# Kernel optimization log

Measured on AMD Instinct MI355X. Metric: run time of the kernel, lower is better.

## Reference

```python
import jax, jax.numpy as jnp
import numpy as np

DT = 0.01  # continuous-time step for the S4D/Vandermonde reservoir kernel


def setup_inputs() -> dict:
    key = jax.random.key(0)
    ks = jax.random.split(key, 10)
    B, H, L, N = 16, 128, 4096, 64
    u = jax.random.normal(ks[0], (B, H, L), dtype=jnp.float32)
    # stable diagonal SSM: real part of Lambda strictly negative
    lambda_re = -0.5 * jax.random.uniform(ks[1], (H, N), dtype=jnp.float32) - 0.1
    lambda_im = jax.random.normal(ks[2], (H, N), dtype=jnp.float32) * np.pi
    w_re = jax.random.normal(ks[3], (H, N), dtype=jnp.float32) / np.sqrt(N)
    w_im = jax.random.normal(ks[4], (H, N), dtype=jnp.float32) / np.sqrt(N)
    d = jax.random.normal(ks[5], (H,), dtype=jnp.float32)
    mlp_w1 = jax.random.normal(ks[6], (H, H), dtype=jnp.float32) / np.sqrt(H)
    mlp_b1 = jnp.zeros((H,), dtype=jnp.float32)
    mlp_w2 = jax.random.normal(ks[7], (H, H), dtype=jnp.float32) / np.sqrt(H)
    mlp_b2 = jnp.zeros((H,), dtype=jnp.float32)
    return {"u": u, "lambda_re": lambda_re, "lambda_im": lambda_im,
            "w_re": w_re, "w_im": w_im, "d": d,
            "mlp_w1": mlp_w1, "mlp_b1": mlp_b1,
            "mlp_w2": mlp_w2, "mlp_b2": mlp_b2}


def reference(u, lambda_re, lambda_im, w_re, w_im, d,
              mlp_w1, mlp_b1, mlp_w2, mlp_b2):
    B, H, L = u.shape
    Lam = lambda_re + 1j * lambda_im          # (H, N) diagonal state matrix
    W = w_re + 1j * w_im                      # (H, N) merged C*B readout
    ell = jnp.arange(L, dtype=jnp.float32)
    # Vandermonde kernel: K[h, l] = sum_n W[h,n] * exp(dt * Lambda[h,n] * l)
    V = jnp.exp((DT * Lam)[:, :, None] * ell[None, None, :])  # (H, N, L)
    K = jnp.einsum('hn,hnl->hl', W, V)                         # (H, L) complex
    # causal FFT convolution (pad to 2L to avoid circular wrap)
    n = 2 * L
    y = jnp.fft.ifft(jnp.fft.fft(u, n=n, axis=-1) * jnp.fft.fft(K, n=n, axis=-1)[None],
                     n=n, axis=-1)[..., :L]
    y = y + d[None, :, None] * u              # skip / feed-through term
    y = y.real                                # Real() projection
    # 1x1-conv MLP with ReLU (mlp_layers = 2)
    h1 = jax.nn.relu(jnp.einsum('oh,bhl->bol', mlp_w1, y) + mlp_b1[None, :, None])
    y2 = jax.nn.relu(jnp.einsum('oh,bhl->bol', mlp_w2, h1) + mlp_b2[None, :, None])
    return y2
```

## Files before the change

### kernel.cpp

```cpp
#include <hip/hip_runtime.h>
#include <hip/hip_bf16.h>

#define B_ 16
#define H_ 128
#define L_ 4096
#define N_ 64
#define DT_ 0.01f

typedef __bf16 bf16;
typedef __bf16 bf16x8 __attribute__((ext_vector_type(8)));
typedef __bf16 bf16x4 __attribute__((ext_vector_type(4)));
typedef float f32x4 __attribute__((ext_vector_type(4)));

__global__ __launch_bounds__(64) void k_prep(
        const float* __restrict__ lre, const float* __restrict__ lim,
        const float* __restrict__ wre, const float* __restrict__ wim,
        const float* __restrict__ w1, const float* __restrict__ w2,
        bf16* __restrict__ w1b, bf16* __restrict__ w2b,
        bf16* __restrict__ Pbf, bf16* __restrict__ Qbf,
        float* __restrict__ tap, float* __restrict__ acre, float* __restrict__ acim) {
    __shared__ bf16  Pl[128 * 72];
    __shared__ bf16  Ql[64 * 136];
    __shared__ float red[64 * 65];

    const int h = blockIdx.x, n = threadIdx.x;

    w1b[h * H_ + n]      = (bf16)w1[h * H_ + n];
    w1b[h * H_ + 64 + n] = (bf16)w1[h * H_ + 64 + n];
    w2b[h * H_ + n]      = (bf16)w2[h * H_ + n];
    w2b[h * H_ + 64 + n] = (bf16)w2[h * H_ + 64 + n];

    const float lr = lre[h * 64 + n] * DT_, li = lim[h * 64 + n] * DT_;
    const float e = expf(lr);
    const float ar = e * cosf(li), ai = e * sinf(li);
    const float wr = wre[h * 64 + n], wi = wim[h * 64 + n];
    const float war = wr * ar - wi * ai;
    const float wai = wr * ai + wi * ar;
    float pr = 1.f, pi = 0.f;
    for (int dlt = 0; dlt < 64; ++dlt) {
        Pl[n * 72 + (63 - dlt)]        = (bf16)pr;
        Pl[(64 + n) * 72 + (63 - dlt)] = (bf16)pi;
        Ql[dlt * 136 + 2 * n]     = (bf16)(war * pr - wai * pi);
        Ql[dlt * 136 + 2 * n + 1] = (bf16)(-(war * pi + wai * pr));
        red[dlt * 65 + n] = wr * pr - wi * pi;
        const float npr = ar * pr - ai * pi;
        const float npi = ar * pi + ai * pr;
        pr = npr; pi = npi;
    }
    acre[h * 64 + n] = pr;
    acim[h * 64 + n] = pi;
    __syncthreads();

    float s = 0.f;
    #pragma unroll
    for (int k = 0; k < 64; ++k) s += red[n * 65 + k];
    tap[h * 64 + n] = s;

    bf16* Ph = Pbf + (size_t)h * 128 * 64;
    bf16* Qh = Qbf + (size_t)h * 64 * 128;
    #pragma unroll
    for (int i = 0; i < 16; ++i) {
        const int flat = i * 512 + n * 8;
        {
            const int row = flat >> 6, col = flat & 63;
            *(bf16x8*)(Ph + flat) = *(const bf16x8*)(&Pl[row * 72 + col]);
        }
        {
            const int row = flat >> 7, col = flat & 127;
            *(bf16x8*)(Qh + flat) = *(const bf16x8*)(&Ql[row * 136 + col]);
        }
    }
}

#define USWZ(c, k) ((c) * 64 + (((((k) >> 4) ^ ((c) & 3)) << 4) | ((k) & 15)))
#define SSWZ(c, k) ((c) * 128 + (((((k) >> 4) ^ ((c) & 7)) << 4) | ((k) & 15)))
__global__ __launch_bounds__(512, 4) void k_ssm2(
        const float* __restrict__ u, const float* __restrict__ dv,
        const bf16* __restrict__ Pbf, const bf16* __restrict__ Qbf,
        const float* __restrict__ tap,
        const float* __restrict__ acre, const float* __restrict__ acim,
        bf16* __restrict__ ybf) {
    __shared__ bf16  Ubf[64 * 64];
    __shared__ float Ctr[128 * 65];
    __shared__ bf16  Sbf[64 * 128];
    __shared__ bf16  Tm[64 * 72];

    const int tid = threadIdx.x;
    const int bh  = blockIdx.x;
    const int h   = bh & (H_ - 1);
    const float* __restrict__ up = u + (size_t)bh * L_;

    {
        const int c = tid >> 3, j0 = (tid & 7) << 3;
        const float4* src = (const float4*)(up + c * 64 + j0);
        float4 f0 = src[0], f1 = src[1];
        bf16x8 t;
        t[0] = (bf16)f0.x; t[1] = (bf16)f0.y; t[2] = (bf16)f0.z; t[3] = (bf16)f0.w;
        t[4] = (bf16)f1.x; t[5] = (bf16)f1.y; t[6] = (bf16)f1.z; t[7] = (bf16)f1.w;
        *(bf16x8*)(&Ubf[USWZ(c, j0)]) = t;
    }
    {
        const int dlt = tid >> 3, j0 = (tid & 7) << 3;
        const float* tp = tap + h * 64;
        const float dh = dv[h];
        bf16x8 t;
        #pragma unroll
        for (int e = 0; e < 8; ++e) {
            const int j = j0 + e;
            float v = (j <= dlt) ? tp[dlt - j] : 0.f;
            if (j == dlt) v += dh;
            t[e] = (bf16)v;
        }
        *(bf16x8*)(&Tm[dlt * 72 + j0]) = t;
    }
    __syncthreads();

    const int lane = tid & 63, wv = tid >> 6;
    const int cl = lane & 15, q = lane >> 4;

    {
        f32x4 acc[4];
        #pragma unroll
        for (int nt = 0; nt < 4; ++nt) acc[nt] = (f32x4){0.f, 0.f, 0.f, 0.f};
        const bf16* Ph = Pbf + (size_t)h * 128 * 64;
        #pragma unroll
        for (int ks = 0; ks < 2; ++ks) {
            const int k0 = ks * 32 + q * 8;
            const bf16x8 a = *(const bf16x8*)(Ph + (size_t)(wv * 16 + cl) * 64 + k0);
            #pragma unroll
            for (int nt = 0; nt < 4; ++nt) {
                const int c = nt * 16 + cl;
                const bf16x8 bfr = *(const bf16x8*)(&Ubf[USWZ(c, k0)]);
                acc[nt] = __builtin_amdgcn_mfma_f32_16x16x32_bf16(a, bfr, acc[nt], 0, 0, 0);
            }
        }
        #pragma unroll
        for (int nt = 0; nt < 4; ++nt)
            #pragma unroll
            for (int r = 0; r < 4; ++r)
                Ctr[(wv * 16 + q * 4 + r) * 65 + nt * 16 + cl] = acc[nt][r];
    }
    __syncthreads();

    if (wv == 0) {
        const int n = lane;
        const float ar = acre[h * 64 + n], ai = acim[h * 64 + n];
        float sr = 0.f, si = 0.f;
        #pragma unroll 8
        for (int c = 0; c < 64; ++c) {
            bf16* sp = &Sbf[SSWZ(c, 2 * n)];
            sp[0] = (bf16)sr;
            sp[1] = (bf16)si;
            const float cr = Ctr[n * 65 + c];
            const float ci = Ctr[(64 + n) * 65 + c];
            const float nr = fmaf(ar, sr, fmaf(-ai, si, cr));
            const float ni = fmaf(ar, si, fmaf(ai, sr, ci));
            sr = nr; si = ni;
        }
    }
    __syncthreads();

    {
        const int mt  = wv >> 1;
        const int nt0 = (wv & 1) * 2;
        f32x4 acc[2];
        acc[0] = (f32x4){0.f, 0.f, 0.f, 0.f};
        acc[1] = (f32x4){0.f, 0.f, 0.f, 0.f};
        const bf16* Qh = Qbf + (size_t)h * 64 * 128;
        #pragma unroll
        for (int ks = 0; ks < 4; ++ks) {
            const int k0 = ks * 32 + q * 8;
            const bf16x8 a = *(const bf16x8*)(Qh + (size_t)(mt * 16 + cl) * 128 + k0);
            #pragma unroll
            for (int j = 0; j < 2; ++j) {
                const int c = (nt0 + j) * 16 + cl;
                const bf16x8 bfr = *(const bf16x8*)(&Sbf[SSWZ(c, k0)]);
                acc[j] = __builtin_amdgcn_mfma_f32_16x16x32_bf16(a, bfr, acc[j], 0, 0, 0);
            }
        }
        #pragma unroll
        for (int ks = 0; ks < 2; ++ks) {
            const int k0 = ks * 32 + q * 8;
            const bf16x8 a = *(const bf16x8*)(&Tm[(mt * 16 + cl) * 72 + k0]);
            #pragma unroll
            for (int j = 0; j < 2; ++j) {
                const int c = (nt0 + j) * 16 + cl;
                const bf16x8 bfr = *(const bf16x8*)(&Ubf[USWZ(c, k0)]);
                acc[j] = __builtin_amdgcn_mfma_f32_16x16x32_bf16(a, bfr, acc[j], 0, 0, 0);
            }
        }
        bf16* Yb = (bf16*)Ctr;
        #pragma unroll
        for (int j = 0; j < 2; ++j) {
            const int c = (nt0 + j) * 16 + cl;
            bf16x4 yv;
            #pragma unroll
            for (int r = 0; r < 4; ++r) yv[r] = (bf16)acc[j][r];
            *(bf16x4*)(&Yb[c * 72 + mt * 16 + q * 4]) = yv;
        }
    }
    __syncthreads();

    {
        const bf16* Yb = (const bf16*)Ctr;
        const int c = tid >> 3, s0 = (tid & 7) << 3;
        bf16x8 v = *(const bf16x8*)(&Yb[c * 72 + s0]);
        *(bf16x8*)(ybf + (size_t)bh * L_ + c * 64 + s0) = v;
    }
}

#define YSTR 136
__global__ __launch_bounds__(256, 4) void k_mlp(
        const bf16* __restrict__ ybf,
        const bf16* __restrict__ w1b, const bf16* __restrict__ w2b,
        const float* __restrict__ b1, const float* __restrict__ b2,
        float* __restrict__ out) {
    __shared__ float Ys[128 * 68];
    __shared__ float B1s[H_], B2s[H_];
    bf16* YT = (bf16*)Ys;

    const int tid = threadIdx.x;
    const int b   = blockIdx.x >> 6;
    const int lt  = blockIdx.x & 63;
    const int l0  = lt * 64;

    if (tid < H_) { B1s[tid] = b1[tid]; B2s[tid] = b2[tid]; }

    {
        const int h  = tid >> 1;
        const int lh = (tid & 1) * 32;
        const bf16x8* src = (const bf16x8*)(ybf + ((size_t)b * H_ + h) * L_ + l0 + lh);
        #pragma unroll
        for (int v = 0; v < 4; ++v) {
            bf16x8 d = src[v];
            #pragma unroll
            for (int e = 0; e < 8; ++e) YT[(lh + v * 8 + e) * YSTR + h] = d[e];
        }
    }
    __syncthreads();

    const int lane = tid & 63;
    const int wv   = tid >> 6;
    const int m    = lane & 15;
    const int q    = lane >> 4;
    const int m0   = wv * 32;

    f32x4 acc[2][4];
    #pragma unroll
    for (int i = 0; i < 2; ++i)
        #pragma unroll
        for (int nt = 0; nt < 4; ++nt) acc[i][nt] = (f32x4){0.f, 0.f, 0.f, 0.f};

    #pragma unroll
    for (int kb = 0; kb < 4; ++kb) {
        const bf16x8 a0 = *(const bf16x8*)(w1b + (size_t)(m0 + m)      * H_ + kb * 32 + q * 8);
        const bf16x8 a1 = *(const bf16x8*)(w1b + (size_t)(m0 + 16 + m) * H_ + kb * 32 + q * 8);
        #pragma unroll
        for (int nt = 0; nt < 4; ++nt) {
            const bf16x8 bfr = *(const bf16x8*)(&YT[(nt * 16 + m) * YSTR + kb * 32 + q * 8]);
            acc[0][nt] = __builtin_amdgcn_mfma_f32_16x16x32_bf16(a0, bfr, acc[0][nt], 0, 0, 0);
            acc[1][nt] = __builtin_amdgcn_mfma_f32_16x16x32_bf16(a1, bfr, acc[1][nt], 0, 0, 0);
        }
    }
    __syncthreads();

    #pragma unroll
    for (int i = 0; i < 2; ++i) {
        const int o0 = m0 + 16 * i + 4 * q;
        #pragma unroll
        for (int nt = 0; nt < 4; ++nt) {
            const f32x4 v = acc[i][nt];
            bf16x4 hv;
            #pragma unroll
            for (int r = 0; r < 4; ++r) {
                float x = v[r] + B1s[o0 + r];
                hv[r] = (bf16)fmaxf(x, 0.f);
            }
            *(bf16x4*)(&YT[(nt * 16 + m) * YSTR + o0]) = hv;
        }
    }
    __syncthreads();

    f32x4 acc2[2][4];
    #pragma unroll
    for (int i = 0; i < 2; ++i)
        #pragma unroll
        for (int nt = 0; nt < 4; ++nt) acc2[i][nt] = (f32x4){0.f, 0.f, 0.f, 0.f};

    #pragma unroll
    for (int kb = 0; kb < 4; ++kb) {
        const bf16x8 a0 = *(const bf16x8*)(w2b + (size_t)(m0 + m)      * H_ + kb * 32 + q * 8);
        const bf16x8 a1 = *(const bf16x8*)(w2b + (size_t)(m0 + 16 + m) * H_ + kb * 32 + q * 8);
        #pragma unroll
        for (int nt = 0; nt < 4; ++nt) {
            const bf16x8 bfr = *(const bf16x8*)(&YT[(nt * 16 + m) * YSTR + kb * 32 + q * 8]);
            acc2[0][nt] = __builtin_amdgcn_mfma_f32_16x16x32_bf16(a0, bfr, acc2[0][nt], 0, 0, 0);
            acc2[1][nt] = __builtin_amdgcn_mfma_f32_16x16x32_bf16(a1, bfr, acc2[1][nt], 0, 0, 0);
        }
    }
    __syncthreads();

    #pragma unroll
    for (int i = 0; i < 2; ++i) {
        const int o0 = m0 + 16 * i + 4 * q;
        #pragma unroll
        for (int nt = 0; nt < 4; ++nt) {
            const f32x4 v = acc2[i][nt];
            #pragma unroll
            for (int r = 0; r < 4; ++r) {
                float x = v[r] + B2s[o0 + r];
                Ys[(o0 + r) * 68 + nt * 16 + m] = fmaxf(x, 0.f);
            }
        }
    }
    __syncthreads();

    {
        const int rg = tid >> 4, c4 = (tid & 15) << 2;
        float* op = out + ((size_t)b * H_) * L_ + l0;
        #pragma unroll
        for (int v = 0; v < 8; ++v) {
            const int row = v * 16 + rg;
            const float4 val = *(const float4*)(&Ys[row * 68 + c4]);
            *(float4*)(op + (size_t)row * L_ + c4) = val;
        }
    }
}

extern "C" void kernel_launch(void* const* d_in, const int* in_sizes, int n_in,
                              void* d_out, int out_size, void* d_ws, size_t ws_size,
                              hipStream_t stream) {
    const float* u   = (const float*)d_in[0];
    const float* lre = (const float*)d_in[1];
    const float* lim = (const float*)d_in[2];
    const float* wre = (const float*)d_in[3];
    const float* wim = (const float*)d_in[4];
    const float* dv  = (const float*)d_in[5];
    const float* w1  = (const float*)d_in[6];
    const float* b1  = (const float*)d_in[7];
    const float* w2  = (const float*)d_in[8];
    const float* b2  = (const float*)d_in[9];
    float* out = (float*)d_out;

    char* ws = (char*)d_ws;
    bf16*  ybf  = (bf16*)ws;                 ws += (size_t)B_ * H_ * L_ * 2;
    bf16*  w1b  = (bf16*)ws;                 ws += H_ * H_ * 2;
    bf16*  w2b  = (bf16*)ws;                 ws += H_ * H_ * 2;
    bf16*  Pbf  = (bf16*)ws;                 ws += (size_t)H_ * 128 * 64 * 2;
    bf16*  Qbf  = (bf16*)ws;                 ws += (size_t)H_ * 64 * 128 * 2;
    float* tap  = (float*)ws;                ws += H_ * 64 * 4;
    float* acre = (float*)ws;                ws += H_ * 64 * 4;
    float* acim = (float*)ws;                ws += H_ * 64 * 4;

    hipLaunchKernelGGL(k_prep, dim3(H_), dim3(64), 0, stream,
                       lre, lim, wre, wim, w1, w2, w1b, w2b,
                       Pbf, Qbf, tap, acre, acim);
    hipLaunchKernelGGL(k_ssm2, dim3(B_ * H_), dim3(512), 0, stream,
                       u, dv, Pbf, Qbf, tap, acre, acim, ybf);
    hipLaunchKernelGGL(k_mlp, dim3(B_ * (L_ / 64)), dim3(256), 0, stream,
                       ybf, w1b, w2b, b1, b2, out);
}
```

Baseline: 138.1 us.

## Fuse SSM prep into main kernel, compute power matrices in registers, loop over batches

Removes the separate k_prep launch. The Vandermonde P/Q fragments, taps and A^64 are now computed directly in registers and shared memory with closed-form exp/sin/cos instead of serial powers. Each block now handles 4 batch elements for one head, so the setup cost is paid once per block, and the bf16 weight conversion is folded into the same kernel. This cuts a launch and the workspace traffic. In exchange the grid shrinks from 2048 to 512 blocks, a serial loop is added per block, and fast-math intrinsics may lose some accuracy.

Result: faster. 131.2 us (-5.0%).

```diff
diff --git a/kernel.cpp b/kernel.cpp
--- a/kernel.cpp
+++ b/kernel.cpp
@@ -12,200 +12,210 @@
 typedef __bf16 bf16x4 __attribute__((ext_vector_type(4)));
 typedef float f32x4 __attribute__((ext_vector_type(4)));
 
-__global__ __launch_bounds__(64) void k_prep(
+#define USWZ(c, k) ((c) * 64 + (((((k) >> 4) ^ ((c) & 3)) << 4) | ((k) & 15)))
+#define SSWZ(c, k) ((c) * 128 + (((((k) >> 4) ^ ((c) & 7)) << 4) | ((k) & 15)))
+
+__global__ __launch_bounds__(512, 4) void k_ssm3(
+        const float* __restrict__ u,
         const float* __restrict__ lre, const float* __restrict__ lim,
         const float* __restrict__ wre, const float* __restrict__ wim,
+        const float* __restrict__ dv,
         const float* __restrict__ w1, const float* __restrict__ w2,
         bf16* __restrict__ w1b, bf16* __restrict__ w2b,
-        bf16* __restrict__ Pbf, bf16* __restrict__ Qbf,
-        float* __restrict__ tap, float* __restrict__ acre, float* __restrict__ acim) {
-    __shared__ bf16  Pl[128 * 72];
-    __shared__ bf16  Ql[64 * 136];
-    __shared__ float red[64 * 65];
-
-    const int h = blockIdx.x, n = threadIdx.x;
-
-    w1b[h * H_ + n]      = (bf16)w1[h * H_ + n];
-    w1b[h * H_ + 64 + n] = (bf16)w1[h * H_ + 64 + n];
-    w2b[h * H_ + n]      = (bf16)w2[h * H_ + n];
-    w2b[h * H_ + 64 + n] = (bf16)w2[h * H_ + 64 + n];
-
-    const float lr = lre[h * 64 + n] * DT_, li = lim[h * 64 + n] * DT_;
-    const float e = expf(lr);
-    const float ar = e * cosf(li), ai = e * sinf(li);
-    const float wr = wre[h * 64 + n], wi = wim[h * 64 + n];
-    const float war = wr * ar - wi * ai;
-    const float wai = wr * ai + wi * ar;
-    float pr = 1.f, pi = 0.f;
-    for (int dlt = 0; dlt < 64; ++dlt) {
-        Pl[n * 72 + (63 - dlt)]        = (bf16)pr;
-        Pl[(64 + n) * 72 + (63 - dlt)] = (bf16)pi;
-        Ql[dlt * 136 + 2 * n]     = (bf16)(war * pr - wai * pi);
-        Ql[dlt * 136 + 2 * n + 1] = (bf16)(-(war * pi + wai * pr));
-        red[dlt * 65 + n] = wr * pr - wi * pi;
-        const float npr = ar * pr - ai * pi;
-        const float npi = ar * pi + ai * pr;
-        pr = npr; pi = npi;
-    }
-    acre[h * 64 + n] = pr;
-    acim[h * 64 + n] = pi;
-    __syncthreads();
-
-    float s = 0.f;
-    #pragma unroll
-    for (int k = 0; k < 64; ++k) s += red[n * 65 + k];
-    tap[h * 64 + n] = s;
-
-    bf16* Ph = Pbf + (size_t)h * 128 * 64;
-    bf16* Qh = Qbf + (size_t)h * 64 * 128;
-    #pragma unroll
-    for (int i = 0; i < 16; ++i) {
-        const int flat = i * 512 + n * 8;
-        {
-            const int row = flat >> 6, col = flat & 63;
-            *(bf16x8*)(Ph + flat) = *(const bf16x8*)(&Pl[row * 72 + col]);
-        }
-        {
-            const int row = flat >> 7, col = flat & 127;
-            *(bf16x8*)(Qh + flat) = *(const bf16x8*)(&Ql[row * 136 + col]);
-        }
-    }
-}
-
-#define USWZ(c, k) ((c) * 64 + (((((k) >> 4) ^ ((c) & 3)) << 4) | ((k) & 15)))
-#define SSWZ(c, k) ((c) * 128 + (((((k) >> 4) ^ ((c) & 7)) << 4) | ((k) & 15)))
-__global__ __launch_bounds__(512, 4) void k_ssm2(
-        const float* __restrict__ u, const float* __restrict__ dv,
-        const bf16* __restrict__ Pbf, const bf16* __restrict__ Qbf,
-        const float* __restrict__ tap,
-        const float* __restrict__ acre, const float* __restrict__ acim,
         bf16* __restrict__ ybf) {
-    __shared__ bf16  Ubf[64 * 64];
-    __shared__ float Ctr[128 * 65];
-    __shared__ bf16  Sbf[64 * 128];
-    __shared__ bf16  Tm[64 * 72];
-
-    const int tid = threadIdx.x;
-    const int bh  = blockIdx.x;
-    const int h   = bh & (H_ - 1);
-    const float* __restrict__ up = u + (size_t)bh * L_;
-
-    {
-        const int c = tid >> 3, j0 = (tid & 7) << 3;
-        const float4* src = (const float4*)(up + c * 64 + j0);
-        float4 f0 = src[0], f1 = src[1];
-        bf16x8 t;
-        t[0] = (bf16)f0.x; t[1] = (bf16)f0.y; t[2] = (bf16)f0.z; t[3] = (bf16)f0.w;
-        t[4] = (bf16)f1.x; t[5] = (bf16)f1.y; t[6] = (bf16)f1.z; t[7] = (bf16)f1.w;
-        *(bf16x8*)(&Ubf[USWZ(c, j0)]) = t;
-    }
+    alignas(16) __shared__ char smem[68352];
+    bf16*  Ubf  = (bf16*)smem;
+    float* Ctr  = (float*)(smem + 8192);
+    bf16*  Sbf  = (bf16*)(smem + 41472);
+    bf16*  Tm   = (bf16*)(smem + 57856);
+    float* lamS = (float*)(smem + 67072);
+    float* taps = (float*)(smem + 68096);
+
+    const int tid  = threadIdx.x;
+    const int lane = tid & 63, wv = tid >> 6;
+    const int cl   = lane & 15, q = lane >> 4;
+    const int bId  = blockIdx.x;
+    const int h    = bId & 127;
+    const int bg   = bId >> 7;
+
+    if (tid < 64) {
+        if (bId < 256) w1b[bId * 64 + tid] = (bf16)w1[bId * 64 + tid];
+        else           w2b[(bId - 256) * 64 + tid] = (bf16)w2[(bId - 256) * 64 + tid];
+    }
+    if (tid < 64) {
+        lamS[tid]       = lre[h * 64 + tid] * DT_;
+        lamS[64 + tid]  = lim[h * 64 + tid] * DT_;
+        lamS[128 + tid] = wre[h * 64 + tid];
+        lamS[192 + tid] = wim[h * 64 + tid];
+    }
+    __syncthreads();
+
+    bf16x8 pA0, pA1;
+    {
+        const int row = wv * 16 + cl;
+        const int n = row & 63;
+        const bool isIm = row >= 64;
+        const float lr = lamS[n], li = lamS[64 + n];
+        #pragma unroll
+        for (int jj = 0; jj < 8; ++jj) {
+            const float p0 = (float)(63 - (q * 8 + jj));
+            const float e0 = __expf(p0 * lr);
+            pA0[jj] = (bf16)(isIm ? e0 * __sinf(p0 * li) : e0 * __cosf(p0 * li));
+            const float p1 = (float)(63 - (32 + q * 8 + jj));
+            const float e1 = __expf(p1 * lr);
+            pA1[jj] = (bf16)(isIm ? e1 * __sinf(p1 * li) : e1 * __cosf(p1 * li));
+        }
+    }
+    bf16x8 qA[4];
+    {
+        const float fd = (float)((wv >> 1) * 16 + cl + 1);
+        #pragma unroll
+        for (int ks = 0; ks < 4; ++ks) {
+            #pragma unroll
+            for (int nn = 0; nn < 4; ++nn) {
+                const int n = ks * 16 + q * 4 + nn;
+                const float lr = lamS[n], li = lamS[64 + n];
+                const float wr = lamS[128 + n], wi = lamS[192 + n];
+                const float e  = __expf(fd * lr);
+                const float cr = e * __cosf(fd * li), ci = e * __sinf(fd * li);
+                qA[ks][2 * nn]     = (bf16)(wr * cr - wi * ci);
+                qA[ks][2 * nn + 1] = (bf16)(-(wr * ci + wi * cr));
+            }
+        }
+    }
+    float a64r, a64i;
+    {
+        const float lr = lamS[lane], li = lamS[64 + lane];
+        const float e = __expf(64.f * lr);
+        a64r = e * __cosf(64.f * li);
+        a64i = e * __sinf(64.f * li);
+    }
+    {
+        const float lr = lamS[lane], li = lamS[64 + lane];
+        const float wr = lamS[128 + lane], wi = lamS[192 + lane];
+        #pragma unroll
+        for (int i = 0; i < 8; ++i) {
+            const int dlt = wv * 8 + i;
+            const float fd = (float)dlt;
+            const float e = __expf(fd * lr);
+            float t = wr * e * __cosf(fd * li) - wi * e * __sinf(fd * li);
+            #pragma unroll
+            for (int d = 1; d < 64; d <<= 1) t += __shfl_xor(t, d, 64);
+            if (lane == 0) taps[dlt] = t;
+        }
+    }
+    __syncthreads();
+
     {
         const int dlt = tid >> 3, j0 = (tid & 7) << 3;
-        const float* tp = tap + h * 64;
         const float dh = dv[h];
         bf16x8 t;
         #pragma unroll
         for (int e = 0; e < 8; ++e) {
             const int j = j0 + e;
-            float v = (j <= dlt) ? tp[dlt - j] : 0.f;
+            float v = (j <= dlt) ? taps[dlt - j] : 0.f;
             if (j == dlt) v += dh;
             t[e] = (bf16)v;
         }
         *(bf16x8*)(&Tm[dlt * 72 + j0]) = t;
     }
-    __syncthreads();
-
-    const int lane = tid & 63, wv = tid >> 6;
-    const int cl = lane & 15, q = lane >> 4;
-
-    {
-        f32x4 acc[4];
-        #pragma unroll
-        for (int nt = 0; nt < 4; ++nt) acc[nt] = (f32x4){0.f, 0.f, 0.f, 0.f};
-        const bf16* Ph = Pbf + (size_t)h * 128 * 64;
-        #pragma unroll
-        for (int ks = 0; ks < 2; ++ks) {
-            const int k0 = ks * 32 + q * 8;
-            const bf16x8 a = *(const bf16x8*)(Ph + (size_t)(wv * 16 + cl) * 64 + k0);
+
+    const int mt = wv >> 1, nt0 = (wv & 1) * 2;
+    for (int it = 0; it < 4; ++it) {
+        const int bh = (bg * 4 + it) * 128 + h;
+        const float* __restrict__ up = u + (size_t)bh * L_;
+
+        {
+            const int c = tid >> 3, j0 = (tid & 7) << 3;
+            const float4* src = (const float4*)(up + c * 64 + j0);
+            const float4 f0 = src[0], f1 = src[1];
+            bf16x8 t;
+            t[0] = (bf16)f0.x; t[1] = (bf16)f0.y; t[2] = (bf16)f0.z; t[3] = (bf16)f0.w;
+            t[4] = (bf16)f1.x; t[5] = (bf16)f1.y; t[6] = (bf16)f1.z; t[7] = (bf16)f1.w;
+            *(bf16x8*)(&Ubf[USWZ(c, j0)]) = t;
+        }
+        __syncthreads();
+
+        {
+            f32x4 acc[4];
+            #pragma unroll
+            for (int nt = 0; nt < 4; ++nt) acc[nt] = (f32x4){0.f, 0.f, 0.f, 0.f};
             #pragma unroll
             for (int nt = 0; nt < 4; ++nt) {
                 const int c = nt * 16 + cl;
-                const bf16x8 bfr = *(const bf16x8*)(&Ubf[USWZ(c, k0)]);
-                acc[nt] = __builtin_amdgcn_mfma_f32_16x16x32_bf16(a, bfr, acc[nt], 0, 0, 0);
-            }
-        }
-        #pragma unroll
-        for (int nt = 0; nt < 4; ++nt)
-            #pragma unroll
-            for (int r = 0; r < 4; ++r)
-                Ctr[(wv * 16 + q * 4 + r) * 65 + nt * 16 + cl] = acc[nt][r];
-    }
-    __syncthreads();
-
-    if (wv == 0) {
-        const int n = lane;
-        const float ar = acre[h * 64 + n], ai = acim[h * 64 + n];
-        float sr = 0.f, si = 0.f;
-        #pragma unroll 8
-        for (int c = 0; c < 64; ++c) {
-            bf16* sp = &Sbf[SSWZ(c, 2 * n)];
-            sp[0] = (bf16)sr;
-            sp[1] = (bf16)si;
-            const float cr = Ctr[n * 65 + c];
-            const float ci = Ctr[(64 + n) * 65 + c];
-            const float nr = fmaf(ar, sr, fmaf(-ai, si, cr));
-            const float ni = fmaf(ar, si, fmaf(ai, sr, ci));
-            sr = nr; si = ni;
-        }
-    }
-    __syncthreads();
-
-    {
-        const int mt  = wv >> 1;
-        const int nt0 = (wv & 1) * 2;
-        f32x4 acc[2];
-        acc[0] = (f32x4){0.f, 0.f, 0.f, 0.f};
-        acc[1] = (f32x4){0.f, 0.f, 0.f, 0.f};
-        const bf16* Qh = Qbf + (size_t)h * 64 * 128;
-        #pragma unroll
-        for (int ks = 0; ks < 4; ++ks) {
-            const int k0 = ks * 32 + q * 8;
-            const bf16x8 a = *(const bf16x8*)(Qh + (size_t)(mt * 16 + cl) * 128 + k0);
+                const bf16x8 b0 = *(const bf16x8*)(&Ubf[USWZ(c, q * 8)]);
+                acc[nt] = __builtin_amdgcn_mfma_f32_16x16x32_bf16(pA0, b0, acc[nt], 0, 0, 0);
+                const bf16x8 bq = *(const bf16x8*)(&Ubf[USWZ(c, 32 + q * 8)]);
+                acc[nt] = __builtin_amdgcn_mfma_f32_16x16x32_bf16(pA1, bq, acc[nt], 0, 0, 0);
+            }
+            #pragma unroll
+            for (int nt = 0; nt < 4; ++nt)
+                #pragma unroll
+                for (int r = 0; r < 4; ++r)
+                    Ctr[(wv * 16 + q * 4 + r) * 65 + nt * 16 + cl] = acc[nt][r];
+        }
+        __syncthreads();
+
+        if (wv == 0) {
+            float sr = 0.f, si = 0.f;
+            #pragma unroll 8
+            for (int c = 0; c < 64; ++c) {
+                bf16* sp = &Sbf[SSWZ(c, 2 * lane)];
+                sp[0] = (bf16)sr;
+                sp[1] = (bf16)si;
+                const float cr = Ctr[lane * 65 + c];
+                const float ci = Ctr[(64 + lane) * 65 + c];
+                const float nr = fmaf(a64r, sr, fmaf(-a64i, si, cr));
+                const float ni = fmaf(a64r, si, fmaf(a64i, sr, ci));
+                sr = nr; si = ni;
+            }
+        }
+        __syncthreads();
+
+        {
+            f32x4 acc[2];
+            acc[0] = (f32x4){0.f, 0.f, 0.f, 0.f};
+            acc[1] = (f32x4){0.f, 0.f, 0.f, 0.f};
+            #pragma unroll
+            for (int ks = 0; ks < 4; ++ks) {
+                const int k0 = ks * 32 + q * 8;
+                #pragma unroll
+                for (int j = 0; j < 2; ++j) {
+                    const int c = (nt0 + j) * 16 + cl;
+                    const bf16x8 bfr = *(const bf16x8*)(&Sbf[SSWZ(c, k0)]);
+                    acc[j] = __builtin_amdgcn_mfma_f32_16x16x32_bf16(qA[ks], bfr, acc[j], 0, 0, 0);
+                }
+            }
+            #pragma unroll
+            for (int ks = 0; ks < 2; ++ks) {
+                const int k0 = ks * 32 + q * 8;
+                const bf16x8 a = *(const bf16x8*)(&Tm[(mt * 16 + cl) * 72 + k0]);
+                #pragma unroll
+                for (int j = 0; j < 2; ++j) {
+                    const int c = (nt0 + j) * 16 + cl;
+                    const bf16x8 bfr = *(const bf16x8*)(&Ubf[USWZ(c, k0)]);
+                    acc[j] = __builtin_amdgcn_mfma_f32_16x16x32_bf16(a, bfr, acc[j], 0, 0, 0);
+                }
+            }
+            bf16* Yb = (bf16*)Ctr;
             #pragma unroll
             for (int j = 0; j < 2; ++j) {
                 const int c = (nt0 + j) * 16 + cl;
-                const bf16x8 bfr = *(const bf16x8*)(&Sbf[SSWZ(c, k0)]);
-                acc[j] = __builtin_amdgcn_mfma_f32_16x16x32_bf16(a, bfr, acc[j], 0, 0, 0);
-            }
-        }
-        #pragma unroll
-        for (int ks = 0; ks < 2; ++ks) {
-            const int k0 = ks * 32 + q * 8;
-            const bf16x8 a = *(const bf16x8*)(&Tm[(mt * 16 + cl) * 72 + k0]);
-            #pragma unroll
-            for (int j = 0; j < 2; ++j) {
-                const int c = (nt0 + j) * 16 + cl;
-                const bf16x8 bfr = *(const bf16x8*)(&Ubf[USWZ(c, k0)]);
-                acc[j] = __builtin_amdgcn_mfma_f32_16x16x32_bf16(a, bfr, acc[j], 0, 0, 0);
-            }
-        }
-        bf16* Yb = (bf16*)Ctr;
-        #pragma unroll
-        for (int j = 0; j < 2; ++j) {
-            const int c = (nt0 + j) * 16 + cl;
-            bf16x4 yv;
-            #pragma unroll
-            for (int r = 0; r < 4; ++r) yv[r] = (bf16)acc[j][r];
-            *(bf16x4*)(&Yb[c * 72 + mt * 16 + q * 4]) = yv;
-        }
-    }
-    __syncthreads();
-
-    {
-        const bf16* Yb = (const bf16*)Ctr;
-        const int c = tid >> 3, s0 = (tid & 7) << 3;
-        bf16x8 v = *(const bf16x8*)(&Yb[c * 72 + s0]);
-        *(bf16x8*)(ybf + (size_t)bh * L_ + c * 64 + s0) = v;
+                bf16x4 yv;
+                #pragma unroll
+                for (int r = 0; r < 4; ++r) yv[r] = (bf16)acc[j][r];
+                *(bf16x4*)(&Yb[c * 72 + mt * 16 + q * 4]) = yv;
+            }
+        }
+        __syncthreads();
+
+        {
+            const bf16* Yb = (const bf16*)Ctr;
+            const int c = tid >> 3, s0 = (tid & 7) << 3;
+            const bf16x8 v = *(const bf16x8*)(&Yb[c * 72 + s0]);
+            *(bf16x8*)(ybf + (size_t)bh * L_ + c * 64 + s0) = v;
+        }
+        __syncthreads();
     }
 }
 
@@ -343,20 +353,12 @@
     float* out = (float*)d_out;
 
     char* ws = (char*)d_ws;
-    bf16*  ybf  = (bf16*)ws;                 ws += (size_t)B_ * H_ * L_ * 2;
-    bf16*  w1b  = (bf16*)ws;                 ws += H_ * H_ * 2;
-    bf16*  w2b  = (bf16*)ws;                 ws += H_ * H_ * 2;
-    bf16*  Pbf  = (bf16*)ws;                 ws += (size_t)H_ * 128 * 64 * 2;
-    bf16*  Qbf  = (bf16*)ws;                 ws += (size_t)H_ * 64 * 128 * 2;
-    float* tap  = (float*)ws;                ws += H_ * 64 * 4;
-    float* acre = (float*)ws;                ws += H_ * 64 * 4;
-    float* acim = (float*)ws;                ws += H_ * 64 * 4;
-
-    hipLaunchKernelGGL(k_prep, dim3(H_), dim3(64), 0, stream,
-                       lre, lim, wre, wim, w1, w2, w1b, w2b,
-                       Pbf, Qbf, tap, acre, acim);
-    hipLaunchKernelGGL(k_ssm2, dim3(B_ * H_), dim3(512), 0, stream,
-                       u, dv, Pbf, Qbf, tap, acre, acim, ybf);
+    bf16* ybf = (bf16*)ws;   ws += (size_t)B_ * H_ * L_ * 2;
+    bf16* w1b = (bf16*)ws;   ws += H_ * H_ * 2;
+    bf16* w2b = (bf16*)ws;   ws += H_ * H_ * 2;
+
+    hipLaunchKernelGGL(k_ssm3, dim3(512), dim3(512), 0, stream,
+                       u, lre, lim, wre, wim, dv, w1, w2, w1b, w2b, ybf);
     hipLaunchKernelGGL(k_mlp, dim3(B_ * (L_ / 64)), dim3(256), 0, stream,
                        ybf, w1b, w2b, b1, b2, out);
 }
```
